# Kernel optimization log

Measured on AMD Instinct MI355X. Metric: run time of the kernel, lower is better.

The kernel has to match this reference:

```python
import jax, jax.numpy as jnp
import numpy as np

THRESHOLD_FACTOR = 1.25

def setup_inputs() -> dict:
    key = jax.random.key(0)
    r_embed = jax.random.normal(key, (2, 4096, 2), dtype=jnp.float32)
    return {"r_embed": r_embed}

def reference(r_embed):
    # r_embed: [b, n, 2]
    # diff[b,s,t,i] = -r[b,s,i]*r[b,t,i] + r[b,s,i]   (einsum('bsi,bti->bsti', r, -r) + r.unsqueeze(2))
    diff = -r_embed[:, :, None, :] * r_embed[:, None, :, :] + r_embed[:, :, None, :]  # [b,s,t,2]
    dist_sq = jnp.sum(diff * diff, axis=-1)                                            # [b,s,t]
    phase_diff = jnp.arctan2(diff[..., 1], diff[..., 0])
    forward_bias = 0.5 * (1.0 + jnp.cos(phase_diff)) * jnp.exp(-dist_sq)
    mean_dist = jnp.mean(dist_sq, axis=(-1, -2), keepdims=True)
    n = dist_sq.shape[-1] * dist_sq.shape[-2]
    # torch.std default is unbiased (divide by n-1)
    var = jnp.sum((dist_sq - mean_dist) ** 2, axis=(-1, -2), keepdims=True) / (n - 1)
    std_dist = jnp.maximum(jnp.sqrt(var), 1e-6)
    threshold = mean_dist + THRESHOLD_FACTOR * std_dist
    valid_mask = (dist_sq <= threshold).astype(dist_sq.dtype)
    attention = valid_mask * forward_bias
    row_sums = jnp.sum(attention, axis=-1, keepdims=True)
    attention = attention / (row_sums + 1e-8)
    return attention
```

## Files before the change

### kernel.cpp

```cpp
#include <hip/hip_runtime.h>
#include <math.h>

#define N 4096
#define NB 2
#define THRESHOLD_FACTOR 1.25

__global__ __launch_bounds__(256) void stats_kernel(const float* __restrict__ r,
                                                    float* __restrict__ thr) {
    int b = blockIdx.x;
    const float2* rb2 = (const float2*)(r + (size_t)b * N * 2);
    int tid = threadIdx.x;

    double s[10];
#pragma unroll
    for (int i = 0; i < 10; ++i) s[i] = 0.0;

    for (int idx = tid; idx < N; idx += 256) {
        float2 p = rb2[idx];
        float x = p.x;
        float y = p.y;
        double a  = (double)x * (double)x;
        double bb = (double)y * (double)y;
        double ax = 1.0 - (double)x;
        double by = 1.0 - (double)y;
        double A  = ax * ax;
        double Bv = by * by;
        s[0] += a;      s[1] += bb;      s[2] += A;      s[3] += Bv;
        s[4] += a * a;  s[5] += bb * bb; s[6] += a * bb;
        s[7] += A * A;  s[8] += Bv * Bv; s[9] += A * Bv;
    }

    __shared__ double red[256][11];
#pragma unroll
    for (int q = 0; q < 10; ++q) red[tid][q] = s[q];
    __syncthreads();
    for (int st = 128; st > 0; st >>= 1) {
        if (tid < st) {
#pragma unroll
            for (int q = 0; q < 10; ++q) red[tid][q] += red[tid + st][q];
        }
        __syncthreads();
    }

    if (tid == 0) {
        double t0 = red[0][0], t1 = red[0][1], t2 = red[0][2], t3 = red[0][3];
        double t4 = red[0][4], t5 = red[0][5], t6 = red[0][6];
        double t7 = red[0][7], t8 = red[0][8], t9 = red[0][9];
        double pairs = (double)N * (double)N;
        double sum_d  = t0 * t2 + t1 * t3;
        double sum_d2 = t4 * t7 + t5 * t8 + 2.0 * t6 * t9;
        double mean = sum_d / pairs;
        double var = (sum_d2 - sum_d * sum_d / pairs) / (pairs - 1.0);
        double sd = sqrt(var);
        if (sd < 1e-6) sd = 1e-6;
        thr[b] = (float)(mean + THRESHOLD_FACTOR * sd);
    }
}

__global__ __launch_bounds__(256) void attn_kernel(const float* __restrict__ r,
                                                   const float* __restrict__ thr,
                                                   float* __restrict__ out) {
    int blk = blockIdx.x;
    int b = blk >> 11;
    int s0 = (blk & 2047) << 1;
    const float* rb = r + (size_t)b * N * 2;

    float4 rs = *(const float4*)(rb + (size_t)s0 * 2);
    float ax = rs.x, ay = rs.y;
    float bx = rs.z, by = rs.w;
    float threshold = thr[b];

    int tid = threadIdx.x;
    float va[16], vb[16];
    float sumA = 0.0f, sumB = 0.0f;

#pragma unroll
    for (int g = 0; g < 4; ++g) {
        int t0 = g * 1024 + tid * 4;
        float4 p0 = *(const float4*)(rb + (size_t)t0 * 2);
        float4 p1 = *(const float4*)(rb + (size_t)t0 * 2 + 4);
        float tx[4] = {p0.x, p0.z, p1.x, p1.z};
        float ty[4] = {p0.y, p0.w, p1.y, p1.w};
#pragma unroll
        for (int k = 0; k < 4; ++k) {
            float dxA = fmaf(-ax, tx[k], ax);
            float dyA = fmaf(-ay, ty[k], ay);
            float dA  = fmaf(dxA, dxA, dyA * dyA);
            float cA  = (dA > 0.0f) ? dxA * __builtin_amdgcn_rsqf(dA) : 1.0f;
            float eA  = 0.5f * __expf(-dA);
            float fbA = fmaf(cA, eA, eA);
            float vA  = (dA <= threshold) ? fbA : 0.0f;
            va[g * 4 + k] = vA;
            sumA += vA;
            float dxB = fmaf(-bx, tx[k], bx);
            float dyB = fmaf(-by, ty[k], by);
            float dB  = fmaf(dxB, dxB, dyB * dyB);
            float cB  = (dB > 0.0f) ? dxB * __builtin_amdgcn_rsqf(dB) : 1.0f;
            float eB  = 0.5f * __expf(-dB);
            float fbB = fmaf(cB, eB, eB);
            float vB  = (dB <= threshold) ? fbB : 0.0f;
            vb[g * 4 + k] = vB;
            sumB += vB;
        }
    }

#pragma unroll
    for (int off = 32; off > 0; off >>= 1) {
        sumA += __shfl_down(sumA, off, 64);
        sumB += __shfl_down(sumB, off, 64);
    }
    __shared__ float wsum[2][4];
    int lane = tid & 63;
    int wid = tid >> 6;
    if (lane == 0) { wsum[0][wid] = sumA; wsum[1][wid] = sumB; }
    __syncthreads();
    float totA = wsum[0][0] + wsum[0][1] + wsum[0][2] + wsum[0][3];
    float totB = wsum[1][0] + wsum[1][1] + wsum[1][2] + wsum[1][3];
    float invA = __builtin_amdgcn_rcpf(totA + 1e-8f);
    float invB = __builtin_amdgcn_rcpf(totB + 1e-8f);

    size_t rowA = ((size_t)b * N + (size_t)s0) * N;
    float4* outA = (float4*)(out + rowA);
    float4* outB = (float4*)(out + rowA + N);
#pragma unroll
    for (int g = 0; g < 4; ++g) {
        int t0 = g * 1024 + tid * 4;
        float4 w4;
        w4.x = va[g * 4 + 0] * invA;
        w4.y = va[g * 4 + 1] * invA;
        w4.z = va[g * 4 + 2] * invA;
        w4.w = va[g * 4 + 3] * invA;
        outA[t0 >> 2] = w4;
        float4 u4;
        u4.x = vb[g * 4 + 0] * invB;
        u4.y = vb[g * 4 + 1] * invB;
        u4.z = vb[g * 4 + 2] * invB;
        u4.w = vb[g * 4 + 3] * invB;
        outB[t0 >> 2] = u4;
    }
}

extern "C" void kernel_launch(void* const* d_in, const int* in_sizes, int n_in,
                              void* d_out, int out_size, void* d_ws, size_t ws_size,
                              hipStream_t stream) {
    const float* r = (const float*)d_in[0];
    float* out = (float*)d_out;
    float* thr = (float*)d_ws;

    stats_kernel<<<NB, 256, 0, stream>>>(r, thr);
    attn_kernel<<<NB * 2048, 256, 0, stream>>>(r, thr, out);
}
```

Before: 145.9 us.

## Split stats reduction across blocks and use nontemporal output stores

The single-block-per-batch statistics kernel becomes a 32-block partial reduction that uses wavefront shuffles, followed by a small final kernel that combines the partials and computes the threshold. This spreads the double-precision statistics work across more CUs and removes the serial shared-memory tree. The attention kernel's output writes become nontemporal vector stores, so the large streaming output does not pollute the caches. The cost is one extra kernel launch and a workspace buffer for the partial sums.

New measurement: 147.0 us. No clear change (+0.8%).

```diff
diff --git a/kernel.cpp b/kernel.cpp
--- a/kernel.cpp
+++ b/kernel.cpp
@@ -4,57 +4,77 @@
 #define N 4096
 #define NB 2
 #define THRESHOLD_FACTOR 1.25
+#define PB 16
 
-__global__ __launch_bounds__(256) void stats_kernel(const float* __restrict__ r,
-                                                    float* __restrict__ thr) {
-    int b = blockIdx.x;
+typedef float floatx4 __attribute__((ext_vector_type(4)));
+
+
+__global__ __launch_bounds__(256) void stats_partial(const float* __restrict__ r,
+                                                     double* __restrict__ part) {
+    int blk = blockIdx.x;
+    int b = blk >> 4;
+    int chunk = blk & 15;
+    int tid = threadIdx.x;
+    int idx = chunk * 256 + tid;
+
     const float2* rb2 = (const float2*)(r + (size_t)b * N * 2);
-    int tid = threadIdx.x;
+    float2 p = rb2[idx];
+    double x = (double)p.x, y = (double)p.y;
+    double a  = x * x;
+    double bb = y * y;
+    double ax = 1.0 - x, by = 1.0 - y;
+    double A  = ax * ax;
+    double Bv = by * by;
+    double s[10] = {a, bb, A, Bv, a * a, bb * bb, a * bb, A * A, Bv * Bv, A * Bv};
 
-    double s[10];
 #pragma unroll
-    for (int i = 0; i < 10; ++i) s[i] = 0.0;
-
-    for (int idx = tid; idx < N; idx += 256) {
-        float2 p = rb2[idx];
-        float x = p.x;
-        float y = p.y;
-        double a  = (double)x * (double)x;
-        double bb = (double)y * (double)y;
-        double ax = 1.0 - (double)x;
-        double by = 1.0 - (double)y;
-        double A  = ax * ax;
-        double Bv = by * by;
-        s[0] += a;      s[1] += bb;      s[2] += A;      s[3] += Bv;
-        s[4] += a * a;  s[5] += bb * bb; s[6] += a * bb;
-        s[7] += A * A;  s[8] += Bv * Bv; s[9] += A * Bv;
+    for (int q = 0; q < 10; ++q) {
+        double v = s[q];
+#pragma unroll
+        for (int off = 32; off > 0; off >>= 1) v += __shfl_down(v, off, 64);
+        s[q] = v;
     }
 
-    __shared__ double red[256][11];
+    __shared__ double wred[4][10];
+    int lane = tid & 63, wid = tid >> 6;
+    if (lane == 0) {
 #pragma unroll
-    for (int q = 0; q < 10; ++q) red[tid][q] = s[q];
+        for (int q = 0; q < 10; ++q) wred[wid][q] = s[q];
+    }
     __syncthreads();
-    for (int st = 128; st > 0; st >>= 1) {
-        if (tid < st) {
+    if (tid == 0) {
 #pragma unroll
-            for (int q = 0; q < 10; ++q) red[tid][q] += red[tid + st][q];
-        }
-        __syncthreads();
+        for (int q = 0; q < 10; ++q)
+            part[(b * 10 + q) * PB + chunk] =
+                wred[0][q] + wred[1][q] + wred[2][q] + wred[3][q];
     }
+}
 
-    if (tid == 0) {
-        double t0 = red[0][0], t1 = red[0][1], t2 = red[0][2], t3 = red[0][3];
-        double t4 = red[0][4], t5 = red[0][5], t6 = red[0][6];
-        double t7 = red[0][7], t8 = red[0][8], t9 = red[0][9];
+__global__ __launch_bounds__(320) void stats_final(const double* __restrict__ part,
+                                                   float* __restrict__ thr) {
+    int tid = threadIdx.x;
+    double v = part[tid];
+#pragma unroll
+    for (int off = 8; off > 0; off >>= 1) v += __shfl_down(v, off, 16);
+    __shared__ double sums[20];
+    if ((tid & 15) == 0) sums[tid >> 4] = v;
+    __syncthreads();
+    if (tid < NB) {
+        const double* t = &sums[tid * 10];
         double pairs = (double)N * (double)N;
-        double sum_d  = t0 * t2 + t1 * t3;
-        double sum_d2 = t4 * t7 + t5 * t8 + 2.0 * t6 * t9;
+        double sum_d  = t[0] * t[2] + t[1] * t[3];
+        double sum_d2 = t[4] * t[7] + t[5] * t[8] + 2.0 * t[6] * t[9];
         double mean = sum_d / pairs;
         double var = (sum_d2 - sum_d * sum_d / pairs) / (pairs - 1.0);
         double sd = sqrt(var);
         if (sd < 1e-6) sd = 1e-6;
-        thr[b] = (float)(mean + THRESHOLD_FACTOR * sd);
+        thr[tid] = (float)(mean + THRESHOLD_FACTOR * sd);
     }
+}
+
+__device__ inline void nt_store4(float* p, float x, float y, float z, float w) {
+    floatx4 v = {x, y, z, w};
+    __builtin_nontemporal_store(v, (floatx4*)p);
 }
 
 __global__ __launch_bounds__(256) void attn_kernel(const float* __restrict__ r,
@@ -120,23 +140,17 @@
     float invB = __builtin_amdgcn_rcpf(totB + 1e-8f);
 
     size_t rowA = ((size_t)b * N + (size_t)s0) * N;
-    float4* outA = (float4*)(out + rowA);
-    float4* outB = (float4*)(out + rowA + N);
+    float* outA = out + rowA;
+    float* outB = out + rowA + N;
 #pragma unroll
     for (int g = 0; g < 4; ++g) {
         int t0 = g * 1024 + tid * 4;
-        float4 w4;
-        w4.x = va[g * 4 + 0] * invA;
-        w4.y = va[g * 4 + 1] * invA;
-        w4.z = va[g * 4 + 2] * invA;
-        w4.w = va[g * 4 + 3] * invA;
-        outA[t0 >> 2] = w4;
-        float4 u4;
-        u4.x = vb[g * 4 + 0] * invB;
-        u4.y = vb[g * 4 + 1] * invB;
-        u4.z = vb[g * 4 + 2] * invB;
-        u4.w = vb[g * 4 + 3] * invB;
-        outB[t0 >> 2] = u4;
+        nt_store4(outA + t0,
+                  va[g * 4 + 0] * invA, va[g * 4 + 1] * invA,
+                  va[g * 4 + 2] * invA, va[g * 4 + 3] * invA);
+        nt_store4(outB + t0,
+                  vb[g * 4 + 0] * invB, vb[g * 4 + 1] * invB,
+                  vb[g * 4 + 2] * invB, vb[g * 4 + 3] * invB);
     }
 }
 
@@ -146,7 +160,9 @@
     const float* r = (const float*)d_in[0];
     float* out = (float*)d_out;
     float* thr = (float*)d_ws;
+    double* part = (double*)((char*)d_ws + 64);
 
-    stats_kernel<<<NB, 256, 0, stream>>>(r, thr);
+    stats_partial<<<NB * PB, 256, 0, stream>>>(r, part);
+    stats_final<<<1, 320, 0, stream>>>(part, thr);
     attn_kernel<<<NB * 2048, 256, 0, stream>>>(r, thr, out);
 }
```
